# Kernel optimization log

Hardware: AMD Instinct MI355X
Metric: run time of the kernel (lower is better)

Reference implementation:

```python
import jax, jax.numpy as jnp
import numpy as np

N_HEADS = 8; N_LEVELS = 4; T_WINDOW = 2; N_CURR = 4; N_TEMP = 2; D_MODEL = 256
D_HEAD = D_MODEL // N_HEADS
SHAPES = [[4, 32, 48], [4, 16, 24], [4, 8, 12], [4, 4, 6]]  # (T, H, W) per level
LEN_IN = sum(t * h * w for t, h, w in SHAPES)  # 8160
LEN_Q = LEN_IN
N_BATCH = 1


def _bilinear_sample(value_l, loc):
    # value_l: (N, M, H, W, D); loc: (N, M, Q, P, 2) normalized to [0, 1].
    # Matches torch grid_sample(mode='bilinear', padding_mode='zeros', align_corners=False)
    # with grid = 2*loc - 1, i.e. pixel coords x = loc_x*W - 0.5, y = loc_y*H - 0.5.
    N, M, H, W, D = value_l.shape
    Q, P = loc.shape[2], loc.shape[3]
    x = loc[..., 0] * W - 0.5
    y = loc[..., 1] * H - 0.5
    x0 = jnp.floor(x); y0 = jnp.floor(y)
    wx = x - x0; wy = y - y0
    flat = value_l.reshape(N, M, H * W, D)

    def gather(xi, yi):
        valid = ((xi >= 0) & (xi < W) & (yi >= 0) & (yi < H)).astype(value_l.dtype)
        idx = (jnp.clip(yi, 0, H - 1) * W + jnp.clip(xi, 0, W - 1)).astype(jnp.int32)
        g = jnp.take_along_axis(flat, idx.reshape(N, M, Q * P, 1), axis=2)
        return g.reshape(N, M, Q, P, D) * valid[..., None]

    v00 = gather(x0, y0); v10 = gather(x0 + 1.0, y0)
    v01 = gather(x0, y0 + 1.0); v11 = gather(x0 + 1.0, y0 + 1.0)
    return (v00 * ((1 - wx) * (1 - wy))[..., None] + v10 * (wx * (1 - wy))[..., None]
            + v01 * ((1 - wx) * wy)[..., None] + v11 * (wx * wy)[..., None])


def _forward(query, reference_points, temporal_offsets, input_flatten, shapes, starts,
             Wv, bv, Ws, bs, Wa, ba, Wts, bts, Wta, bta, Wo, bo):
    N, Lq, _ = query.shape
    value = (input_flatten @ Wv + bv).reshape(N, -1, N_HEADS, D_HEAD)
    ts_off = (query @ Wts + bts).reshape(N, Lq, N_HEADS, N_LEVELS, T_WINDOW, N_TEMP, 2)
    t_attn = (query @ Wta + bta).reshape(N, Lq, N_HEADS, N_LEVELS * T_WINDOW * N_TEMP)
    c_attn = (query @ Wa + ba).reshape(N, Lq, N_HEADS, N_LEVELS * N_CURR)
    # joint softmax over current + temporal sampling points (as in the source)
    attn = jax.nn.softmax(jnp.concatenate([c_attn, t_attn], axis=-1), axis=-1)
    aw_c = attn[..., :N_LEVELS * N_CURR].reshape(N, Lq, N_HEADS, N_LEVELS, N_CURR)
    aw_t = attn[..., N_LEVELS * N_CURR:].reshape(N, Lq, N_HEADS, N_LEVELS, T_WINDOW * N_TEMP)
    aw = jnp.concatenate([aw_c, aw_t], axis=4)  # (N, Lq, M, L, P)
    c_off = (query @ Ws + bs).reshape(N, Lq, N_HEADS, N_LEVELS, N_CURR, 2)
    # flattened-temporal grid per level: width W_l, height T_l*H_l
    norm = jnp.array([[w, t * h] for t, h, w in shapes], dtype=query.dtype)  # (L, 2)
    loc_c = reference_points[:, :, None, :, None, :] + c_off / norm[None, None, None, :, None, :]
    loc_t = (reference_points[:, :, None, :, None, None, :]
             + temporal_offsets[:, :, None, :, :, None, :]
             + ts_off / norm[None, None, None, :, None, None, :])
    loc_t = loc_t.reshape(N, Lq, N_HEADS, N_LEVELS, T_WINDOW * N_TEMP, 2)
    locs = jnp.concatenate([loc_c, loc_t], axis=4)  # (N, Lq, M, L, P, 2)
    out = jnp.zeros((N, N_HEADS, Lq, D_HEAD), query.dtype)
    for l, (t, h, w) in enumerate(shapes):
        s = starts[l]
        vl = value[:, s:s + t * h * w].transpose(0, 2, 1, 3).reshape(N, N_HEADS, t * h, w, D_HEAD)
        loc_l = locs[:, :, :, l].transpose(0, 2, 1, 3, 4)   # (N, M, Lq, P, 2)
        sampled = _bilinear_sample(vl, loc_l)               # (N, M, Lq, P, Dh)
        w_l = aw[:, :, :, l].transpose(0, 2, 1, 3)          # (N, M, Lq, P)
        out = out + jnp.einsum('nmqpd,nmqp->nmqd', sampled, w_l)
    out = out.transpose(0, 2, 1, 3).reshape(N, Lq, D_MODEL)
    return out @ Wo + bo


def setup_inputs() -> dict:
    key = jax.random.key(0)
    ks = jax.random.split(key, 18)
    D = D_MODEL
    sc = 0.02
    query = jax.random.normal(ks[0], (N_BATCH, LEN_Q, D), jnp.float32)
    reference_points = jax.random.uniform(ks[1], (N_BATCH, LEN_Q, N_LEVELS, 2), jnp.float32)
    temporal_offsets = jax.random.uniform(ks[2], (N_BATCH, LEN_Q, N_LEVELS, T_WINDOW, 2),
                                          jnp.float32, minval=-0.25, maxval=0.25)
    input_flatten = jax.random.normal(ks[3], (N_BATCH, LEN_IN, D), jnp.float32)
    input_spatial_shapes = jnp.array(SHAPES, dtype=jnp.int32)
    starts = np.cumsum([0] + [t * h * w for t, h, w in SHAPES])[:-1]
    input_level_start_index = jnp.array(starts, dtype=jnp.int32)
    n_off = N_HEADS * N_LEVELS * N_CURR * 2          # 256
    n_att = N_HEADS * N_LEVELS * N_CURR              # 128
    n_toff = N_HEADS * N_LEVELS * T_WINDOW * N_TEMP * 2  # 256
    n_tatt = N_HEADS * N_LEVELS * T_WINDOW * N_TEMP      # 128
    return {
        'query': query, 'reference_points': reference_points,
        'temporal_offsets': temporal_offsets, 'input_flatten': input_flatten,
        'input_spatial_shapes': input_spatial_shapes,
        'input_level_start_index': input_level_start_index,
        'Wv': jax.random.normal(ks[4], (D, D), jnp.float32) * sc,
        'bv': jnp.zeros((D,), jnp.float32),
        'Ws': jax.random.normal(ks[5], (D, n_off), jnp.float32) * sc,
        'bs': jax.random.normal(ks[6], (n_off,), jnp.float32) * 2.0,
        'Wa': jax.random.normal(ks[7], (D, n_att), jnp.float32) * sc,
        'ba': jnp.zeros((n_att,), jnp.float32),
        'Wts': jax.random.normal(ks[8], (D, n_toff), jnp.float32) * sc,
        'bts': jax.random.normal(ks[9], (n_toff,), jnp.float32) * 2.0,
        'Wta': jax.random.normal(ks[10], (D, n_tatt), jnp.float32) * sc,
        'bta': jnp.zeros((n_tatt,), jnp.float32),
        'Wo': jax.random.normal(ks[11], (D, D), jnp.float32) * sc,
        'bo': jnp.zeros((D,), jnp.float32),
    }


def reference(query, reference_points, temporal_offsets, input_flatten,
              input_spatial_shapes, input_level_start_index,
              Wv, bv, Ws, bs, Wa, ba, Wts, bts, Wta, bta, Wo, bo):
    shapes = [tuple(int(v) for v in row) for row in np.asarray(input_spatial_shapes)]
    starts = [int(v) for v in np.asarray(input_level_start_index)]
    return _forward(query, reference_points, temporal_offsets, input_flatten,
                    shapes, starts, Wv, bv, Ws, bs, Wa, ba, Wts, bts, Wta, bta, Wo, bo)
```

## Files before the change

### kernel.cpp

```cpp
#include <hip/hip_runtime.h>


#define LEN 8160
#define NCONV (2 * LEN * 256)
#define NPACK (1280 * 256)

typedef __attribute__((ext_vector_type(8))) short bf16x8;
typedef __attribute__((ext_vector_type(4))) float f32x4;

__device__ __forceinline__ void split_bf16(float v, unsigned short* hi, unsigned short* lo)
{
    unsigned u = __float_as_uint(v);
    unsigned r = (u + 0x7FFFu + ((u >> 16) & 1u)) & 0xFFFF0000u;
    float hif = __uint_as_float(r);
    float lof = v - hif;
    unsigned ul = __float_as_uint(lof);
    unsigned rl = (ul + 0x7FFFu + ((ul >> 16) & 1u)) >> 16;
    *hi = (unsigned short)(r >> 16);
    *lo = (unsigned short)rl;
}

__global__ __launch_bounds__(256) void prep_kernel(
    const float* __restrict__ inpf, const float* __restrict__ query,
    const float* __restrict__ Ws, const float* __restrict__ bs,
    const float* __restrict__ Wa, const float* __restrict__ ba,
    const float* __restrict__ Wts, const float* __restrict__ bts,
    const float* __restrict__ Wta, const float* __restrict__ bta,
    const float* __restrict__ Wv, const float* __restrict__ Wo,
    unsigned short* __restrict__ Ahi, unsigned short* __restrict__ Alo,
    unsigned short* __restrict__ Qhi, unsigned short* __restrict__ Qlo,
    unsigned short* __restrict__ Whi, unsigned short* __restrict__ Wlo,
    float* __restrict__ bcat)
{
    int idx = blockIdx.x * 256 + threadIdx.x;
    if (idx < NCONV) {
        int which = (idx >= LEN * 256) ? 1 : 0;
        int off = idx - which * (LEN * 256);
        float v = which ? query[off] : inpf[off];
        unsigned short h, l; split_bf16(v, &h, &l);
        if (which) { Qhi[off] = h; Qlo[off] = l; }
        else       { Ahi[off] = h; Alo[off] = l; }
    } else if (idx < NCONV + NPACK) {
        int j2 = idx - NCONV;
        int n = j2 >> 8, k = j2 & 255;
        float v;
        if (n < 256) v = Wv[k * 256 + n];
        else if (n < 1024) {
            int j = n - 256;
            if (j < 256)      v = Ws [k * 256 + j];
            else if (j < 384) v = Wa [k * 128 + (j - 256)];
            else if (j < 640) v = Wts[k * 256 + (j - 384)];
            else              v = Wta[k * 128 + (j - 640)];
        } else v = Wo[k * 256 + (n - 1024)];
        unsigned short h, l; split_bf16(v, &h, &l);
        Whi[j2] = h; Wlo[j2] = l;
    } else if (idx < NCONV + NPACK + 768) {
        int j = idx - (NCONV + NPACK);
        float v;
        if (j < 256)      v = bs[j];
        else if (j < 384) v = ba[j - 256];
        else if (j < 640) v = bts[j - 384];
        else              v = bta[j - 640];
        bcat[j] = v;
    }
}

__global__ __launch_bounds__(256) void gemm_mfma_dual(
    const unsigned short* __restrict__ A0hi, const unsigned short* __restrict__ A0lo,
    const unsigned short* __restrict__ B0hi, const unsigned short* __restrict__ B0lo,
    const float* __restrict__ bias0, float* __restrict__ C0, int N0, int nbx0,
    const unsigned short* __restrict__ A1hi, const unsigned short* __restrict__ A1lo,
    const unsigned short* __restrict__ B1hi, const unsigned short* __restrict__ B1lo,
    const float* __restrict__ bias1, float* __restrict__ C1, int N1)
{
    __shared__ unsigned short BsH[64][72];
    __shared__ unsigned short BsL[64][72];
    const int tid = threadIdx.x;
    const int wave = tid >> 6, lane = tid & 63;
    int bx = blockIdx.x;
    const int by = blockIdx.y;

    const unsigned short *Ahi, *Alo, *Bhi, *Blo;
    const float* bias; float* C; int N;
    if (bx < nbx0) {
        Ahi = A0hi; Alo = A0lo; Bhi = B0hi; Blo = B0lo;
        bias = bias0; C = C0; N = N0;
    } else {
        bx -= nbx0;
        Ahi = A1hi; Alo = A1lo; Bhi = B1hi; Blo = B1lo;
        bias = bias1; C = C1; N = N1;
    }

    const int lm = lane & 15;
    const int kq = lane >> 4;

    const int m = by * 64 + wave * 16 + lm;
    const unsigned short* aHp = Ahi + (size_t)m * 256 + kq * 8;
    const unsigned short* aLp = Alo + (size_t)m * 256 + kq * 8;

    const int sn = tid >> 2;
    const int sk = (tid & 3) * 16;
    const unsigned short* bHs = Bhi + (size_t)(bx * 64 + sn) * 256 + sk;
    const unsigned short* bLs = Blo + (size_t)(bx * 64 + sn) * 256 + sk;

    f32x4 acc[4] = {};
    for (int kc = 0; kc < 4; kc++) {
        *(uint4*)(&BsH[sn][sk])     = *(const uint4*)(bHs + kc * 64);
        *(uint4*)(&BsH[sn][sk + 8]) = *(const uint4*)(bHs + kc * 64 + 8);
        *(uint4*)(&BsL[sn][sk])     = *(const uint4*)(bLs + kc * 64);
        *(uint4*)(&BsL[sn][sk + 8]) = *(const uint4*)(bLs + kc * 64 + 8);
        __syncthreads();
        #pragma unroll
        for (int kt = 0; kt < 2; kt++) {
            const int ko = kc * 64 + kt * 32;
            bf16x8 ah = *(const bf16x8*)(aHp + ko);
            bf16x8 al = *(const bf16x8*)(aLp + ko);
            #pragma unroll
            for (int nt = 0; nt < 4; nt++) {
                bf16x8 bh = *(const bf16x8*)(&BsH[nt * 16 + lm][kt * 32 + kq * 8]);
                bf16x8 bl = *(const bf16x8*)(&BsL[nt * 16 + lm][kt * 32 + kq * 8]);
                acc[nt] = __builtin_amdgcn_mfma_f32_16x16x32_bf16(ah, bh, acc[nt], 0, 0, 0);
                acc[nt] = __builtin_amdgcn_mfma_f32_16x16x32_bf16(ah, bl, acc[nt], 0, 0, 0);
                acc[nt] = __builtin_amdgcn_mfma_f32_16x16x32_bf16(al, bh, acc[nt], 0, 0, 0);
            }
        }
        __syncthreads();
    }
    const int row0 = by * 64 + wave * 16 + kq * 4;
    const int col = bx * 64 + lm;
    #pragma unroll
    for (int nt = 0; nt < 4; nt++) {
        float bb = bias[col + nt * 16];
        #pragma unroll
        for (int r = 0; r < 4; r++) {
            int row = row0 + r;
            if (row < LEN)
                C[(size_t)row * N + col + nt * 16] = acc[nt][r] + bb;
        }
    }
}

__global__ __launch_bounds__(256) void sample_kernel(
    const float* __restrict__ value,
    const float* __restrict__ proj,
    const float* __restrict__ refp,
    const float* __restrict__ toff,
    unsigned short* __restrict__ attn_hi,
    unsigned short* __restrict__ attn_lo)
{
    const int q = blockIdx.x;
    const int head = threadIdx.x >> 5;
    const int lane = threadIdx.x & 31;
    __shared__ int4   s_idx[8][32];
    __shared__ float4 s_w[8][32];

    const float* p = proj + (size_t)q * 768;

    {
        const int i = lane;
        float logit, ox, oy, rx, ry;
        int l;
        if (i < 16) {
            l = i >> 2; int pt2 = i & 3;
            logit = p[256 + head * 16 + i];
            ox = p[head * 32 + l * 8 + pt2 * 2 + 0];
            oy = p[head * 32 + l * 8 + pt2 * 2 + 1];
            rx = refp[q * 8 + l * 2 + 0];
            ry = refp[q * 8 + l * 2 + 1];
        } else {
            int j = i - 16; l = j >> 2;
            int tp = j & 3, tw = tp >> 1, nt = tp & 1;
            logit = p[640 + head * 16 + j];
            ox = p[384 + head * 32 + l * 8 + tw * 4 + nt * 2 + 0];
            oy = p[384 + head * 32 + l * 8 + tw * 4 + nt * 2 + 1];
            rx = refp[q * 8 + l * 2 + 0] + toff[q * 16 + l * 4 + tw * 2 + 0];
            ry = refp[q * 8 + l * 2 + 1] + toff[q * 16 + l * 4 + tw * 2 + 1];
        }
        const int Wl = 48 >> l;
        const int Hgl = 128 >> l;
        const int st = 8192 - (8192 >> (2 * l));
        const float fW = (float)Wl, fHg = (float)Hgl;
        float x = (rx + ox / fW) * fW - 0.5f;
        float y = (ry + oy / fHg) * fHg - 0.5f;

        float mx = logit;
        #pragma unroll
        for (int off = 16; off > 0; off >>= 1)
            mx = fmaxf(mx, __shfl_xor(mx, off, 32));
        float e = expf(logit - mx);
        float s = e;
        #pragma unroll
        for (int off = 16; off > 0; off >>= 1)
            s += __shfl_xor(s, off, 32);
        float w = e / s;

        float fx = floorf(x), fy = floorf(y);
        float wx = x - fx, wy = y - fy;
        int x0 = (int)fx, y0 = (int)fy;
        int x1 = x0 + 1, y1 = y0 + 1;
        float m00 = ((unsigned)x0 < (unsigned)Wl && (unsigned)y0 < (unsigned)Hgl) ? 1.f : 0.f;
        float m10 = ((unsigned)x1 < (unsigned)Wl && (unsigned)y0 < (unsigned)Hgl) ? 1.f : 0.f;
        float m01 = ((unsigned)x0 < (unsigned)Wl && (unsigned)y1 < (unsigned)Hgl) ? 1.f : 0.f;
        float m11 = ((unsigned)x1 < (unsigned)Wl && (unsigned)y1 < (unsigned)Hgl) ? 1.f : 0.f;
        int cx0 = min(max(x0, 0), Wl - 1), cx1 = min(max(x1, 0), Wl - 1);
        int cy0 = min(max(y0, 0), Hgl - 1), cy1 = min(max(y1, 0), Hgl - 1);
        int4 ii;
        ii.x = (st + cy0 * Wl + cx0) * 64;
        ii.y = (st + cy0 * Wl + cx1) * 64;
        ii.z = (st + cy1 * Wl + cx0) * 64;
        ii.w = (st + cy1 * Wl + cx1) * 64;
        float sx0 = 1.f - wx, sy0 = 1.f - wy;
        float4 ww;
        ww.x = w * sx0 * sy0 * m00;
        ww.y = w * wx  * sy0 * m10;
        ww.z = w * sx0 * wy  * m01;
        ww.w = w * wx  * wy  * m11;
        s_idx[head][lane] = ii;
        s_w[head][lane] = ww;
    }
    __syncthreads();

    const int pt4 = lane >> 3;
    const int c4  = lane & 7;
    const float4* vb = (const float4*)value + head * 8 + c4;
    float4 acc = make_float4(0.f, 0.f, 0.f, 0.f);
    #pragma unroll 4
    for (int i = 0; i < 8; i++) {
        int pidx = (i << 2) | pt4;
        int4 ii = s_idx[head][pidx];
        float4 ww = s_w[head][pidx];
        float4 v0 = vb[ii.x], v1 = vb[ii.y], v2 = vb[ii.z], v3 = vb[ii.w];
        acc.x = fmaf(ww.x, v0.x, acc.x); acc.y = fmaf(ww.x, v0.y, acc.y);
        acc.z = fmaf(ww.x, v0.z, acc.z); acc.w = fmaf(ww.x, v0.w, acc.w);
        acc.x = fmaf(ww.y, v1.x, acc.x); acc.y = fmaf(ww.y, v1.y, acc.y);
        acc.z = fmaf(ww.y, v1.z, acc.z); acc.w = fmaf(ww.y, v1.w, acc.w);
        acc.x = fmaf(ww.z, v2.x, acc.x); acc.y = fmaf(ww.z, v2.y, acc.y);
        acc.z = fmaf(ww.z, v2.z, acc.z); acc.w = fmaf(ww.z, v2.w, acc.w);
        acc.x = fmaf(ww.w, v3.x, acc.x); acc.y = fmaf(ww.w, v3.y, acc.y);
        acc.z = fmaf(ww.w, v3.z, acc.z); acc.w = fmaf(ww.w, v3.w, acc.w);
    }
    #pragma unroll
    for (int off = 8; off <= 16; off <<= 1) {
        acc.x += __shfl_xor(acc.x, off, 32);
        acc.y += __shfl_xor(acc.y, off, 32);
        acc.z += __shfl_xor(acc.z, off, 32);
        acc.w += __shfl_xor(acc.w, off, 32);
    }
    if (pt4 == 0) {
        unsigned short h0, l0, h1, l1, h2, l2, h3, l3;
        split_bf16(acc.x, &h0, &l0); split_bf16(acc.y, &h1, &l1);
        split_bf16(acc.z, &h2, &l2); split_bf16(acc.w, &h3, &l3);
        uint2 hv, lv;
        hv.x = (unsigned)h0 | ((unsigned)h1 << 16);
        hv.y = (unsigned)h2 | ((unsigned)h3 << 16);
        lv.x = (unsigned)l0 | ((unsigned)l1 << 16);
        lv.y = (unsigned)l2 | ((unsigned)l3 << 16);
        size_t o = (size_t)q * 256 + head * 32 + c4 * 4;
        *(uint2*)(attn_hi + o) = hv;
        *(uint2*)(attn_lo + o) = lv;
    }
}

extern "C" void kernel_launch(void* const* d_in, const int* in_sizes, int n_in,
                              void* d_out, int out_size, void* d_ws, size_t ws_size,
                              hipStream_t stream)
{
    const float* query = (const float*)d_in[0];
    const float* refp  = (const float*)d_in[1];
    const float* toff  = (const float*)d_in[2];
    const float* inpf  = (const float*)d_in[3];
    const float* Wv  = (const float*)d_in[6];
    const float* bv  = (const float*)d_in[7];
    const float* Ws_ = (const float*)d_in[8];
    const float* bs_ = (const float*)d_in[9];
    const float* Wa  = (const float*)d_in[10];
    const float* ba  = (const float*)d_in[11];
    const float* Wts = (const float*)d_in[12];
    const float* bts = (const float*)d_in[13];
    const float* Wta = (const float*)d_in[14];
    const float* bta = (const float*)d_in[15];
    const float* Wo  = (const float*)d_in[16];
    const float* bo  = (const float*)d_in[17];
    float* out = (float*)d_out;

    float* ws    = (float*)d_ws;
    float* value = ws;
    float* proj  = value + (size_t)LEN * 256;
    float* bcat  = proj + (size_t)LEN * 768;
    unsigned short* Whi = (unsigned short*)(bcat + 768);
    unsigned short* Wlo = Whi + 1280 * 256;
    unsigned short* Ahi = Wlo + 1280 * 256;
    unsigned short* Alo = Ahi + 8192 * 256;
    unsigned short* Qhi = Alo + 8192 * 256;
    unsigned short* Qlo = Qhi + 8192 * 256;

    dim3 blk(256);
    prep_kernel<<<17603, blk, 0, stream>>>(inpf, query, Ws_, bs_, Wa, ba,
                                           Wts, bts, Wta, bta, Wv, Wo,
                                           Ahi, Alo, Qhi, Qlo, Whi, Wlo, bcat);
    gemm_mfma_dual<<<dim3(16, 128), blk, 0, stream>>>(
        Ahi, Alo, Whi, Wlo, bv, value, 256, 4,
        Qhi, Qlo, Whi + 256 * 256, Wlo + 256 * 256, bcat, proj, 768);
    sample_kernel<<<LEN, blk, 0, stream>>>(value, proj, refp, toff, Ahi, Alo);
    gemm_mfma_dual<<<dim3(4, 128), blk, 0, stream>>>(
        Ahi, Alo, Whi + 1024 * 256, Wlo + 1024 * 256, bo, out, 256, 4,
        Ahi, Alo, Whi + 1024 * 256, Wlo + 1024 * 256, bo, out, 256);
}
```

Measured before the change: 188.0 us.

## Retile GEMM with full-K LDS B tile, bf16 value storage, vectorized prep and sampling

The prep kernel now converts and packs eight elements per thread with 128-bit loads and stores. The GEMM becomes a 512-thread block covering 256 rows that loads the whole K=256 B tile into LDS once in MFMA fragment order, removing the per-chunk barriers and reusing each B fragment across two row tiles. The value projection is written as single bf16 instead of fp32, which halves the bytes the sampling kernel gathers. The sampler then loads 8 bf16 channels per gather. Storing value in bf16 drops the low-part correction, so precision is lower.

```diff
diff --git a/kernel.cpp b/kernel.cpp
--- a/kernel.cpp
+++ b/kernel.cpp
@@ -2,11 +2,18 @@
 
 
 #define LEN 8160
-#define NCONV (2 * LEN * 256)
-#define NPACK (1280 * 256)
+#define NCONV8 (2 * LEN * 256 / 8)
+#define NPACK8 (1280 * 256 / 8)
 
 typedef __attribute__((ext_vector_type(8))) short bf16x8;
+typedef __attribute__((ext_vector_type(8))) unsigned short u16x8;
 typedef __attribute__((ext_vector_type(4))) float f32x4;
+
+__device__ __forceinline__ unsigned short rne_bf16(float v)
+{
+    unsigned u = __float_as_uint(v);
+    return (unsigned short)((u + 0x7FFFu + ((u >> 16) & 1u)) >> 16);
+}
 
 __device__ __forceinline__ void split_bf16(float v, unsigned short* hi, unsigned short* lo)
 {
@@ -18,6 +25,11 @@
     unsigned rl = (ul + 0x7FFFu + ((ul >> 16) & 1u)) >> 16;
     *hi = (unsigned short)(r >> 16);
     *lo = (unsigned short)rl;
+}
+
+__device__ __forceinline__ float bf2f(unsigned short s)
+{
+    return __uint_as_float(((unsigned)s) << 16);
 }
 
 __global__ __launch_bounds__(256) void prep_kernel(
@@ -33,29 +45,52 @@
     float* __restrict__ bcat)
 {
     int idx = blockIdx.x * 256 + threadIdx.x;
-    if (idx < NCONV) {
-        int which = (idx >= LEN * 256) ? 1 : 0;
-        int off = idx - which * (LEN * 256);
-        float v = which ? query[off] : inpf[off];
-        unsigned short h, l; split_bf16(v, &h, &l);
-        if (which) { Qhi[off] = h; Qlo[off] = l; }
-        else       { Ahi[off] = h; Alo[off] = l; }
-    } else if (idx < NCONV + NPACK) {
-        int j2 = idx - NCONV;
-        int n = j2 >> 8, k = j2 & 255;
-        float v;
-        if (n < 256) v = Wv[k * 256 + n];
-        else if (n < 1024) {
-            int j = n - 256;
-            if (j < 256)      v = Ws [k * 256 + j];
-            else if (j < 384) v = Wa [k * 128 + (j - 256)];
-            else if (j < 640) v = Wts[k * 256 + (j - 384)];
-            else              v = Wta[k * 128 + (j - 640)];
-        } else v = Wo[k * 256 + (n - 1024)];
-        unsigned short h, l; split_bf16(v, &h, &l);
-        Whi[j2] = h; Wlo[j2] = l;
-    } else if (idx < NCONV + NPACK + 768) {
-        int j = idx - (NCONV + NPACK);
+    if (idx < NCONV8) {
+        int which = (idx >= NCONV8 / 2) ? 1 : 0;
+        int off = (idx - which * (NCONV8 / 2)) * 8;
+        const float* src = which ? query : inpf;
+        float4 a = *(const float4*)(src + off);
+        float4 b = *(const float4*)(src + off + 4);
+        unsigned short h[8], l[8];
+        split_bf16(a.x, &h[0], &l[0]); split_bf16(a.y, &h[1], &l[1]);
+        split_bf16(a.z, &h[2], &l[2]); split_bf16(a.w, &h[3], &l[3]);
+        split_bf16(b.x, &h[4], &l[4]); split_bf16(b.y, &h[5], &l[5]);
+        split_bf16(b.z, &h[6], &l[6]); split_bf16(b.w, &h[7], &l[7]);
+        uint4 hv, lv;
+        hv.x = h[0] | ((unsigned)h[1] << 16); hv.y = h[2] | ((unsigned)h[3] << 16);
+        hv.z = h[4] | ((unsigned)h[5] << 16); hv.w = h[6] | ((unsigned)h[7] << 16);
+        lv.x = l[0] | ((unsigned)l[1] << 16); lv.y = l[2] | ((unsigned)l[3] << 16);
+        lv.z = l[4] | ((unsigned)l[5] << 16); lv.w = l[6] | ((unsigned)l[7] << 16);
+        if (which) { *(uint4*)(Qhi + off) = hv; *(uint4*)(Qlo + off) = lv; }
+        else       { *(uint4*)(Ahi + off) = hv; *(uint4*)(Alo + off) = lv; }
+    } else if (idx < NCONV8 + NPACK8) {
+        int j8 = idx - NCONV8;
+        int n = j8 >> 5;
+        int k0 = (j8 & 31) << 3;
+        unsigned short h[8], l[8];
+        #pragma unroll
+        for (int t = 0; t < 8; t++) {
+            int k = k0 + t;
+            float v;
+            if (n < 256) v = Wv[k * 256 + n];
+            else if (n < 1024) {
+                int j = n - 256;
+                if (j < 256)      v = Ws [k * 256 + j];
+                else if (j < 384) v = Wa [k * 128 + (j - 256)];
+                else if (j < 640) v = Wts[k * 256 + (j - 384)];
+                else              v = Wta[k * 128 + (j - 640)];
+            } else v = Wo[k * 256 + (n - 1024)];
+            split_bf16(v, &h[t], &l[t]);
+        }
+        uint4 hv, lv;
+        hv.x = h[0] | ((unsigned)h[1] << 16); hv.y = h[2] | ((unsigned)h[3] << 16);
+        hv.z = h[4] | ((unsigned)h[5] << 16); hv.w = h[6] | ((unsigned)h[7] << 16);
+        lv.x = l[0] | ((unsigned)l[1] << 16); lv.y = l[2] | ((unsigned)l[3] << 16);
+        lv.z = l[4] | ((unsigned)l[5] << 16); lv.w = l[6] | ((unsigned)l[7] << 16);
+        *(uint4*)(Whi + n * 256 + k0) = hv;
+        *(uint4*)(Wlo + n * 256 + k0) = lv;
+    } else if (idx < NCONV8 + NPACK8 + 768) {
+        int j = idx - (NCONV8 + NPACK8);
         float v;
         if (j < 256)      v = bs[j];
         else if (j < 384) v = ba[j - 256];
@@ -65,83 +100,90 @@
     }
 }
 
-__global__ __launch_bounds__(256) void gemm_mfma_dual(
+__global__ __launch_bounds__(512) void gemm_mfma_dual(
     const unsigned short* __restrict__ A0hi, const unsigned short* __restrict__ A0lo,
     const unsigned short* __restrict__ B0hi, const unsigned short* __restrict__ B0lo,
-    const float* __restrict__ bias0, float* __restrict__ C0, int N0, int nbx0,
+    const float* __restrict__ bias0, void* __restrict__ C0, int N0, int mode0, int nbx0,
     const unsigned short* __restrict__ A1hi, const unsigned short* __restrict__ A1lo,
     const unsigned short* __restrict__ B1hi, const unsigned short* __restrict__ B1lo,
-    const float* __restrict__ bias1, float* __restrict__ C1, int N1)
-{
-    __shared__ unsigned short BsH[64][72];
-    __shared__ unsigned short BsL[64][72];
+    const float* __restrict__ bias1, void* __restrict__ C1, int N1, int mode1)
+{
+    __shared__ unsigned short Bf[2 * 8 * 4 * 64 * 8];
     const int tid = threadIdx.x;
     const int wave = tid >> 6, lane = tid & 63;
     int bx = blockIdx.x;
     const int by = blockIdx.y;
 
     const unsigned short *Ahi, *Alo, *Bhi, *Blo;
-    const float* bias; float* C; int N;
+    const float* bias; void* C; int N, mode;
     if (bx < nbx0) {
         Ahi = A0hi; Alo = A0lo; Bhi = B0hi; Blo = B0lo;
-        bias = bias0; C = C0; N = N0;
+        bias = bias0; C = C0; N = N0; mode = mode0;
     } else {
         bx -= nbx0;
         Ahi = A1hi; Alo = A1lo; Bhi = B1hi; Blo = B1lo;
-        bias = bias1; C = C1; N = N1;
-    }
+        bias = bias1; C = C1; N = N1; mode = mode1;
+    }
+
+    #pragma unroll
+    for (int t = 0; t < 8; t++) {
+        int f = t * 512 + tid;
+        int ln = f & 63, nt = (f >> 6) & 3, kt = (f >> 8) & 7, pl = f >> 11;
+        const unsigned short* src = (pl ? Blo : Bhi)
+            + (size_t)(bx * 64 + nt * 16 + (ln & 15)) * 256 + kt * 32 + (ln >> 4) * 8;
+        *(uint4*)(&Bf[(size_t)f * 8]) = *(const uint4*)src;
+    }
+    __syncthreads();
 
     const int lm = lane & 15;
     const int kq = lane >> 4;
-
-    const int m = by * 64 + wave * 16 + lm;
-    const unsigned short* aHp = Ahi + (size_t)m * 256 + kq * 8;
-    const unsigned short* aLp = Alo + (size_t)m * 256 + kq * 8;
-
-    const int sn = tid >> 2;
-    const int sk = (tid & 3) * 16;
-    const unsigned short* bHs = Bhi + (size_t)(bx * 64 + sn) * 256 + sk;
-    const unsigned short* bLs = Blo + (size_t)(bx * 64 + sn) * 256 + sk;
-
-    f32x4 acc[4] = {};
-    for (int kc = 0; kc < 4; kc++) {
-        *(uint4*)(&BsH[sn][sk])     = *(const uint4*)(bHs + kc * 64);
-        *(uint4*)(&BsH[sn][sk + 8]) = *(const uint4*)(bHs + kc * 64 + 8);
-        *(uint4*)(&BsL[sn][sk])     = *(const uint4*)(bLs + kc * 64);
-        *(uint4*)(&BsL[sn][sk + 8]) = *(const uint4*)(bLs + kc * 64 + 8);
-        __syncthreads();
-        #pragma unroll
-        for (int kt = 0; kt < 2; kt++) {
-            const int ko = kc * 64 + kt * 32;
-            bf16x8 ah = *(const bf16x8*)(aHp + ko);
-            bf16x8 al = *(const bf16x8*)(aLp + ko);
+    const int m0 = by * 256 + wave * 32 + lm;
+    const unsigned short* aH0 = Ahi + (size_t)m0 * 256 + kq * 8;
+    const unsigned short* aL0 = Alo + (size_t)m0 * 256 + kq * 8;
+
+    f32x4 acc[2][4] = {};
+    #pragma unroll
+    for (int kt = 0; kt < 8; kt++) {
+        bf16x8 ah0 = *(const bf16x8*)(aH0 + kt * 32);
+        bf16x8 al0 = *(const bf16x8*)(aL0 + kt * 32);
+        bf16x8 ah1 = *(const bf16x8*)(aH0 + 16 * 256 + kt * 32);
+        bf16x8 al1 = *(const bf16x8*)(aL0 + 16 * 256 + kt * 32);
+        #pragma unroll
+        for (int nt = 0; nt < 4; nt++) {
+            const int fb = (kt * 4 + nt) * 64 + lane;
+            bf16x8 bh = *(const bf16x8*)(&Bf[(size_t)fb * 8]);
+            bf16x8 bl = *(const bf16x8*)(&Bf[(size_t)(fb + 2048) * 8]);
+            acc[0][nt] = __builtin_amdgcn_mfma_f32_16x16x32_bf16(ah0, bh, acc[0][nt], 0, 0, 0);
+            acc[0][nt] = __builtin_amdgcn_mfma_f32_16x16x32_bf16(ah0, bl, acc[0][nt], 0, 0, 0);
+            acc[0][nt] = __builtin_amdgcn_mfma_f32_16x16x32_bf16(al0, bh, acc[0][nt], 0, 0, 0);
+            acc[1][nt] = __builtin_amdgcn_mfma_f32_16x16x32_bf16(ah1, bh, acc[1][nt], 0, 0, 0);
+            acc[1][nt] = __builtin_amdgcn_mfma_f32_16x16x32_bf16(ah1, bl, acc[1][nt], 0, 0, 0);
+            acc[1][nt] = __builtin_amdgcn_mfma_f32_16x16x32_bf16(al1, bh, acc[1][nt], 0, 0, 0);
+        }
+    }
+
+    const int col = bx * 64 + lm;
+    #pragma unroll
+    for (int sub = 0; sub < 2; sub++) {
+        const int row0 = by * 256 + wave * 32 + sub * 16 + kq * 4;
+        #pragma unroll
+        for (int nt = 0; nt < 4; nt++) {
+            float bb = bias[col + nt * 16];
             #pragma unroll
-            for (int nt = 0; nt < 4; nt++) {
-                bf16x8 bh = *(const bf16x8*)(&BsH[nt * 16 + lm][kt * 32 + kq * 8]);
-                bf16x8 bl = *(const bf16x8*)(&BsL[nt * 16 + lm][kt * 32 + kq * 8]);
-                acc[nt] = __builtin_amdgcn_mfma_f32_16x16x32_bf16(ah, bh, acc[nt], 0, 0, 0);
-                acc[nt] = __builtin_amdgcn_mfma_f32_16x16x32_bf16(ah, bl, acc[nt], 0, 0, 0);
-                acc[nt] = __builtin_amdgcn_mfma_f32_16x16x32_bf16(al, bh, acc[nt], 0, 0, 0);
+            for (int r = 0; r < 4; r++) {
+                int row = row0 + r;
+                if (row < LEN) {
+                    float v = acc[sub][nt][r] + bb;
+                    if (mode) ((unsigned short*)C)[(size_t)row * N + col + nt * 16] = rne_bf16(v);
+                    else      ((float*)C)[(size_t)row * N + col + nt * 16] = v;
+                }
             }
         }
-        __syncthreads();
-    }
-    const int row0 = by * 64 + wave * 16 + kq * 4;
-    const int col = bx * 64 + lm;
-    #pragma unroll
-    for (int nt = 0; nt < 4; nt++) {
-        float bb = bias[col + nt * 16];
-        #pragma unroll
-        for (int r = 0; r < 4; r++) {
-            int row = row0 + r;
-            if (row < LEN)
-                C[(size_t)row * N + col + nt * 16] = acc[nt][r] + bb;
-        }
     }
 }
 
 __global__ __launch_bounds__(256) void sample_kernel(
-    const float* __restrict__ value,
+    const unsigned short* __restrict__ value,
     const float* __restrict__ proj,
     const float* __restrict__ refp,
     const float* __restrict__ toff,
@@ -205,10 +247,10 @@
         int cx0 = min(max(x0, 0), Wl - 1), cx1 = min(max(x1, 0), Wl - 1);
         int cy0 = min(max(y0, 0), Hgl - 1), cy1 = min(max(y1, 0), Hgl - 1);
         int4 ii;
-        ii.x = (st + cy0 * Wl + cx0) * 64;
-        ii.y = (st + cy0 * Wl + cx1) * 64;
-        ii.z = (st + cy1 * Wl + cx0) * 64;
-        ii.w = (st + cy1 * Wl + cx1) * 64;
+        ii.x = (st + cy0 * Wl + cx0) * 512;
+        ii.y = (st + cy0 * Wl + cx1) * 512;
+        ii.z = (st + cy1 * Wl + cx0) * 512;
+        ii.w = (st + cy1 * Wl + cx1) * 512;
         float sx0 = 1.f - wx, sy0 = 1.f - wy;
         float4 ww;
         ww.x = w * sx0 * sy0 * m00;
@@ -220,44 +262,45 @@
     }
     __syncthreads();
 
-    const int pt4 = lane >> 3;
-    const int c4  = lane & 7;
-    const float4* vb = (const float4*)value + head * 8 + c4;
-    float4 acc = make_float4(0.f, 0.f, 0.f, 0.f);
-    #pragma unroll 4
-    for (int i = 0; i < 8; i++) {
-        int pidx = (i << 2) | pt4;
+    const int pt8 = lane >> 2;
+    const int cg  = lane & 3;
+    const char* vbase = (const char*)value + head * 64 + cg * 16;
+    float acc[8] = {0.f, 0.f, 0.f, 0.f, 0.f, 0.f, 0.f, 0.f};
+    #pragma unroll
+    for (int i = 0; i < 4; i++) {
+        int pidx = (i << 3) | pt8;
         int4 ii = s_idx[head][pidx];
         float4 ww = s_w[head][pidx];
-        float4 v0 = vb[ii.x], v1 = vb[ii.y], v2 = vb[ii.z], v3 = vb[ii.w];
-        acc.x = fmaf(ww.x, v0.x, acc.x); acc.y = fmaf(ww.x, v0.y, acc.y);
-        acc.z = fmaf(ww.x, v0.z, acc.z); acc.w = fmaf(ww.x, v0.w, acc.w);
-        acc.x = fmaf(ww.y, v1.x, acc.x); acc.y = fmaf(ww.y, v1.y, acc.y);
-        acc.z = fmaf(ww.y, v1.z, acc.z); acc.w = fmaf(ww.y, v1.w, acc.w);
-        acc.x = fmaf(ww.z, v2.x, acc.x); acc.y = fmaf(ww.z, v2.y, acc.y);
-        acc.z = fmaf(ww.z, v2.z, acc.z); acc.w = fmaf(ww.z, v2.w, acc.w);
-        acc.x = fmaf(ww.w, v3.x, acc.x); acc.y = fmaf(ww.w, v3.y, acc.y);
-        acc.z = fmaf(ww.w, v3.z, acc.z); acc.w = fmaf(ww.w, v3.w, acc.w);
-    }
-    #pragma unroll
-    for (int off = 8; off <= 16; off <<= 1) {
-        acc.x += __shfl_xor(acc.x, off, 32);
-        acc.y += __shfl_xor(acc.y, off, 32);
-        acc.z += __shfl_xor(acc.z, off, 32);
-        acc.w += __shfl_xor(acc.w, off, 32);
-    }
-    if (pt4 == 0) {
-        unsigned short h0, l0, h1, l1, h2, l2, h3, l3;
-        split_bf16(acc.x, &h0, &l0); split_bf16(acc.y, &h1, &l1);
-        split_bf16(acc.z, &h2, &l2); split_bf16(acc.w, &h3, &l3);
-        uint2 hv, lv;
-        hv.x = (unsigned)h0 | ((unsigned)h1 << 16);
-        hv.y = (unsigned)h2 | ((unsigned)h3 << 16);
-        lv.x = (unsigned)l0 | ((unsigned)l1 << 16);
-        lv.y = (unsigned)l2 | ((unsigned)l3 << 16);
-        size_t o = (size_t)q * 256 + head * 32 + c4 * 4;
-        *(uint2*)(attn_hi + o) = hv;
-        *(uint2*)(attn_lo + o) = lv;
+        u16x8 v0 = *(const u16x8*)(vbase + ii.x);
+        u16x8 v1 = *(const u16x8*)(vbase + ii.y);
+        u16x8 v2 = *(const u16x8*)(vbase + ii.z);
+        u16x8 v3 = *(const u16x8*)(vbase + ii.w);
+        #pragma unroll
+        for (int j = 0; j < 8; j++) {
+            acc[j] = fmaf(ww.x, bf2f(v0[j]), acc[j]);
+            acc[j] = fmaf(ww.y, bf2f(v1[j]), acc[j]);
+            acc[j] = fmaf(ww.z, bf2f(v2[j]), acc[j]);
+            acc[j] = fmaf(ww.w, bf2f(v3[j]), acc[j]);
+        }
+    }
+    #pragma unroll
+    for (int off = 4; off <= 16; off <<= 1)
+        #pragma unroll
+        for (int j = 0; j < 8; j++)
+            acc[j] += __shfl_xor(acc[j], off, 32);
+
+    if (pt8 == 0) {
+        unsigned short h[8], l[8];
+        #pragma unroll
+        for (int j = 0; j < 8; j++) split_bf16(acc[j], &h[j], &l[j]);
+        uint4 hv, lv;
+        hv.x = h[0] | ((unsigned)h[1] << 16); hv.y = h[2] | ((unsigned)h[3] << 16);
+        hv.z = h[4] | ((unsigned)h[5] << 16); hv.w = h[6] | ((unsigned)h[7] << 16);
+        lv.x = l[0] | ((unsigned)l[1] << 16); lv.y = l[2] | ((unsigned)l[3] << 16);
+        lv.z = l[4] | ((unsigned)l[5] << 16); lv.w = l[6] | ((unsigned)l[7] << 16);
+        size_t o = (size_t)q * 256 + head * 32 + cg * 8;
+        *(uint4*)(attn_hi + o) = hv;
+        *(uint4*)(attn_lo + o) = lv;
     }
 }
 
@@ -283,26 +326,24 @@
     const float* bo  = (const float*)d_in[17];
     float* out = (float*)d_out;
 
-    float* ws    = (float*)d_ws;
-    float* value = ws;
-    float* proj  = value + (size_t)LEN * 256;
-    float* bcat  = proj + (size_t)LEN * 768;
+    unsigned short* value_bf = (unsigned short*)d_ws;
+    float* proj = (float*)(value_bf + (size_t)LEN * 256);
+    float* bcat = proj + (size_t)LEN * 768;
     unsigned short* Whi = (unsigned short*)(bcat + 768);
     unsigned short* Wlo = Whi + 1280 * 256;
     unsigned short* Ahi = Wlo + 1280 * 256;
-    unsigned short* Alo = Ahi + 8192 * 256;
-    unsigned short* Qhi = Alo + 8192 * 256;
-    unsigned short* Qlo = Qhi + 8192 * 256;
-
-    dim3 blk(256);
-    prep_kernel<<<17603, blk, 0, stream>>>(inpf, query, Ws_, bs_, Wa, ba,
-                                           Wts, bts, Wta, bta, Wv, Wo,
-                                           Ahi, Alo, Qhi, Qlo, Whi, Wlo, bcat);
-    gemm_mfma_dual<<<dim3(16, 128), blk, 0, stream>>>(
-        Ahi, Alo, Whi, Wlo, bv, value, 256, 4,
-        Qhi, Qlo, Whi + 256 * 256, Wlo + 256 * 256, bcat, proj, 768);
-    sample_kernel<<<LEN, blk, 0, stream>>>(value, proj, refp, toff, Ahi, Alo);
-    gemm_mfma_dual<<<dim3(4, 128), blk, 0, stream>>>(
-        Ahi, Alo, Whi + 1024 * 256, Wlo + 1024 * 256, bo, out, 256, 4,
-        Ahi, Alo, Whi + 1024 * 256, Wlo + 1024 * 256, bo, out, 256);
-}
+    unsigned short* Alo = Ahi + (size_t)8192 * 256;
+    unsigned short* Qhi = Alo + (size_t)8192 * 256;
+    unsigned short* Qlo = Qhi + (size_t)8192 * 256;
+
+    prep_kernel<<<2203, 256, 0, stream>>>(inpf, query, Ws_, bs_, Wa, ba,
+                                          Wts, bts, Wta, bta, Wv, Wo,
+                                          Ahi, Alo, Qhi, Qlo, Whi, Wlo, bcat);
+    gemm_mfma_dual<<<dim3(16, 32), 512, 0, stream>>>(
+        Ahi, Alo, Whi, Wlo, bv, value_bf, 256, 1, 4,
+        Qhi, Qlo, Whi + 256 * 256, Wlo + 256 * 256, bcat, proj, 768, 0);
+    sample_kernel<<<LEN, 256, 0, stream>>>(value_bf, proj, refp, toff, Ahi, Alo);
+    gemm_mfma_dual<<<dim3(4, 32), 512, 0, stream>>>(
+        Ahi, Alo, Whi + 1024 * 256, Wlo + 1024 * 256, bo, out, 256, 0, 4,
+        Ahi, Alo, Whi + 1024 * 256, Wlo + 1024 * 256, bo, out, 256, 0);
+}
```

Result: no change. 184.9 us (-1.6%).
